# Kernel optimization log

Hardware: AMD Instinct MI355X
Metric: run time of the kernel (lower is better)

Reference implementation:

```python
import jax, jax.numpy as jnp
import numpy as np

E = 512; NH = 8; P = 4; Q = 900; CAMS = 7; DEPTH = 4
GRID = (480, 1440); IMG = (1080, 1920); FH = 68; FW = 120
NEG = -1e9  # stand-in for -inf in masked attention (avoids NaN on fully-masked rows)


def _ln(x, g, b):
    m = x.mean(-1, keepdims=True)
    v = jnp.mean((x - m) ** 2, -1, keepdims=True)
    return (x - m) / jnp.sqrt(v + 1e-5) * g + b


def _mlp2(x, w1, b1, w2, b2):
    return jax.nn.relu(x @ w1.T + b1) @ w2.T + b2


def _inv_sig(x, eps=1e-5):
    x = jnp.clip(x, 0.0, 1.0)
    return jnp.log(jnp.clip(x, eps, None) / jnp.clip(1.0 - x, eps, None))


def _mha(x, in_w, in_b, out_w, out_b, nh, mask=None):
    # x: [B, L, E]; mask: bool [B, nh, L, S], True = disallowed (torch semantics)
    B, L, Edim = x.shape
    d = Edim // nh
    qkv = x @ in_w.T + in_b
    q, k, v = jnp.split(qkv, 3, axis=-1)
    q = q.reshape(B, L, nh, d); k = k.reshape(B, L, nh, d); v = v.reshape(B, L, nh, d)
    s = jnp.einsum('blhd,bshd->bhls', q, k) * (1.0 / d ** 0.5)
    if mask is not None:
        s = jnp.where(mask, NEG, s)
    a = jax.nn.softmax(s, -1)
    o = jnp.einsum('bhls,bshd->blhd', a, v).reshape(B, L, Edim)
    return o @ out_w.T + out_b


def _grid_sample(feat, grid):
    # torch.F.grid_sample, bilinear, align_corners=False, zero padding
    # feat: [N, C, H, W], grid: [N, Pn, 2] in [-1, 1] -> [N, C, Pn]
    N, C, H, W = feat.shape
    x = (grid[..., 0] + 1.0) * (W / 2.0) - 0.5
    y = (grid[..., 1] + 1.0) * (H / 2.0) - 0.5
    x0f = jnp.floor(x); y0f = jnp.floor(y)
    wx1 = x - x0f; wy1 = y - y0f
    x0 = x0f.astype(jnp.int32); y0 = y0f.astype(jnp.int32)

    def gat(f, yi, xi):
        ok = ((yi >= 0) & (yi < H) & (xi >= 0) & (xi < W)).astype(f.dtype)
        return f[:, jnp.clip(yi, 0, H - 1), jnp.clip(xi, 0, W - 1)] * ok[None]

    def one(f, x0, y0, wx1, wy1):
        x1 = x0 + 1; y1 = y0 + 1
        wx0 = 1.0 - wx1; wy0 = 1.0 - wy1
        return (gat(f, y0, x0) * (wy0 * wx0)[None] + gat(f, y0, x1) * (wy0 * wx1)[None]
                + gat(f, y1, x0) * (wy1 * wx0)[None] + gat(f, y1, x1) * (wy1 * wx1)[None])

    return jax.vmap(one)(feat, x0, y0, wx1, wy1)


def _forward(img_feats, proj_mat, query, query_pos, reference_points, mha_in_w, mha_in_b, mha_out_w, mha_out_b, off_w1, off_b1, off_w2, off_b2, am_w1, am_b1, am_w2, am_b2, t_ln1_g, t_ln1_b, t_in_w, t_in_b, t_out_w, t_out_b, t_ln2_g, t_ln2_b, t_ff_w1, t_ff_b1, t_ff_w2, t_ff_b2, ffn_w1, ffn_b1, ffn_w2, ffn_b2, op_w, op_b, pe_w1, pe_bias1, pe_ln1_g, pe_ln1_b, pe_w2, pe_bias2, pe_ln2_g, pe_ln2_b, ln1_g, ln1_b, ln2_g, ln2_b, ln3_g, ln3_b):
    q = query + query_pos                                     # [Q, E]
    a = _mha(q[None], mha_in_w, mha_in_b, mha_out_w, mha_out_b, NH)[0]
    qn = _ln(a + q, ln1_g, ln1_b)
    offset = _mlp2(qn, off_w1, off_b1, off_w2, off_b2).reshape(-1, 2)   # [Q*P, 2]
    # torch: inverse_sigmoid(ref).repeat(4,1) + offset  (tile semantics preserved)
    rp_d = jax.nn.sigmoid(jnp.tile(_inv_sig(reference_points), (P, 1)) + offset)
    attn_w = jax.nn.softmax(_mlp2(qn, am_w1, am_b1, am_w2, am_b2), axis=-1)  # [Q, P]

    # --- feature_sampling ---
    scale = jnp.array([GRID[0], GRID[1]], rp_d.dtype)
    pts = jnp.concatenate([rp_d * scale, jnp.ones((Q * P, 1), rp_d.dtype)], -1)  # [Q*P, 3]
    ic = jnp.einsum('nij,pj->npi', proj_mat[0], pts)          # [CAMS, Q*P, 3]
    z = ic[..., 2]
    xy = ic[..., :2] / jnp.maximum(z, 1e-5)[..., None]
    cam = jnp.stack([(xy[..., 0] / IMG[1] - 0.5) * 2.0,
                     (xy[..., 1] / IMG[0] - 0.5) * 2.0], -1)  # [CAMS, Q*P, 2]
    valid = (z > 1e-5) & (cam[..., 0] > -1) & (cam[..., 0] < 1) & (cam[..., 1] > -1) & (cam[..., 1] < 1)
    mask = valid.reshape(CAMS, 1, Q, P).transpose(3, 2, 1, 0)  # [P, Q, 1, CAMS]
    sampled = _grid_sample(img_feats, cam)                    # [CAMS, E, Q*P]
    x = jnp.nan_to_num(sampled.transpose(2, 0, 1))            # [Q*P, CAMS, E]

    inv = ~mask
    m = jnp.tile(jnp.tile(inv, (1, NH, 1, 1)), (1, 1, CAMS, 1)).reshape(-1, CAMS, CAMS)
    mask4 = m.reshape(Q * P, NH, CAMS, CAMS)  # torch (batch*heads, L, S) layout

    for i in range(DEPTH):  # ImgFeatureTransformer, depth=4
        a = _mha(_ln(x, t_ln1_g[i], t_ln1_b[i]), t_in_w[i], t_in_b[i], t_out_w[i], t_out_b[i], NH, mask4)
        x = a + x
        x = _mlp2(_ln(x, t_ln2_g[i], t_ln2_b[i]), t_ff_w1[i], t_ff_b1[i], t_ff_w2[i], t_ff_b2[i]) + x

    out = (x.mean(1).reshape(Q, P, E) * attn_w[:, :, None]).mean(1) @ op_w.T + op_b
    pe = jax.nn.relu(_ln(_inv_sig(reference_points) @ pe_w1.T + pe_bias1, pe_ln1_g, pe_ln1_b))
    pe = jax.nn.relu(_ln(pe @ pe_w2.T + pe_bias2, pe_ln2_g, pe_ln2_b))
    qf = _ln(out + qn + pe, ln2_g, ln2_b)
    return _ln(_mlp2(qf, ffn_w1, ffn_b1, ffn_w2, ffn_b2) + qf, ln3_g, ln3_b)


def setup_inputs() -> dict:
    key = jax.random.key(0)
    ks = iter(jax.random.split(key, 80))
    def nrm(shape, s=1.0):
        return jax.random.normal(next(ks), shape, jnp.float32) * s
    def xw(shape):
        s = (2.0 / (shape[-1] + shape[-2])) ** 0.5
        return nrm(shape, s)
    rng = np.random.RandomState(0)
    base = np.array([[4.0, 0.0, 0.0], [0.0, 0.75, 0.0], [0.0, 0.0, 1.0]], np.float32)
    mats = []
    for _ in range(CAMS):
        M = base.copy()
        M[:2, :2] *= (1.0 + 0.1 * rng.randn(2, 2)).astype(np.float32)
        M[:2, 2] = (50.0 * rng.randn(2)).astype(np.float32)
        M[2, :2] = (1e-4 * rng.randn(2)).astype(np.float32)
        mats.append(M)
    return dict(
        img_feats=nrm((CAMS, E, FH, FW)),
        proj_mat=jnp.asarray(np.stack(mats))[None],
        query=nrm((Q, E), 0.1),
        query_pos=nrm((Q, E), 0.1),
        reference_points=jax.random.uniform(next(ks), (Q, 2), jnp.float32),
        mha_in_w=xw((3 * E, E)), mha_in_b=jnp.zeros((3 * E,)),
        mha_out_w=xw((E, E)), mha_out_b=jnp.zeros((E,)),
        off_w1=xw((E, E)), off_b1=jnp.zeros((E,)), off_w2=xw((2 * P, E)), off_b2=jnp.zeros((2 * P,)),
        am_w1=xw((E, E)), am_b1=jnp.zeros((E,)), am_w2=xw((P, E)), am_b2=jnp.zeros((P,)),
        t_ln1_g=jnp.ones((DEPTH, E)), t_ln1_b=jnp.zeros((DEPTH, E)),
        t_in_w=xw((DEPTH, 3 * E, E)), t_in_b=jnp.zeros((DEPTH, 3 * E)),
        t_out_w=xw((DEPTH, E, E)), t_out_b=jnp.zeros((DEPTH, E)),
        t_ln2_g=jnp.ones((DEPTH, E)), t_ln2_b=jnp.zeros((DEPTH, E)),
        t_ff_w1=xw((DEPTH, E, E)), t_ff_b1=jnp.zeros((DEPTH, E)),
        t_ff_w2=xw((DEPTH, E, E)), t_ff_b2=jnp.zeros((DEPTH, E)),
        ffn_w1=xw((E, E)), ffn_b1=jnp.zeros((E,)), ffn_w2=xw((E, E)), ffn_b2=jnp.zeros((E,)),
        op_w=xw((E, E)), op_b=jnp.zeros((E,)),
        pe_w1=xw((E, 2)), pe_bias1=jnp.zeros((E,)), pe_ln1_g=jnp.ones((E,)), pe_ln1_b=jnp.zeros((E,)),
        pe_w2=xw((E, E)), pe_bias2=jnp.zeros((E,)), pe_ln2_g=jnp.ones((E,)), pe_ln2_b=jnp.zeros((E,)),
        ln1_g=jnp.ones((E,)), ln1_b=jnp.zeros((E,)),
        ln2_g=jnp.ones((E,)), ln2_b=jnp.zeros((E,)),
        ln3_g=jnp.ones((E,)), ln3_b=jnp.zeros((E,)),
    )


def reference(img_feats, proj_mat, query, query_pos, reference_points, mha_in_w, mha_in_b, mha_out_w, mha_out_b, off_w1, off_b1, off_w2, off_b2, am_w1, am_b1, am_w2, am_b2, t_ln1_g, t_ln1_b, t_in_w, t_in_b, t_out_w, t_out_b, t_ln2_g, t_ln2_b, t_ff_w1, t_ff_b1, t_ff_w2, t_ff_b2, ffn_w1, ffn_b1, ffn_w2, ffn_b2, op_w, op_b, pe_w1, pe_bias1, pe_ln1_g, pe_ln1_b, pe_w2, pe_bias2, pe_ln2_g, pe_ln2_b, ln1_g, ln1_b, ln2_g, ln2_b, ln3_g, ln3_b):
    return _forward(img_feats, proj_mat, query, query_pos, reference_points, mha_in_w, mha_in_b, mha_out_w, mha_out_b, off_w1, off_b1, off_w2, off_b2, am_w1, am_b1, am_w2, am_b2, t_ln1_g, t_ln1_b, t_in_w, t_in_b, t_out_w, t_out_b, t_ln2_g, t_ln2_b, t_ff_w1, t_ff_b1, t_ff_w2, t_ff_b2, ffn_w1, ffn_b1, ffn_w2, ffn_b2, op_w, op_b, pe_w1, pe_bias1, pe_ln1_g, pe_ln1_b, pe_w2, pe_bias2, pe_ln2_g, pe_ln2_b, ln1_g, ln1_b, ln2_g, ln2_b, ln3_g, ln3_b)
```

## Files before the change

kernel.cpp:

```cpp
#include <hip/hip_runtime.h>
#include <hip/hip_bf16.h>

#define DEVI __device__ __forceinline__

typedef __bf16 bf16x8 __attribute__((ext_vector_type(8)));
typedef float f32x4 __attribute__((ext_vector_type(4)));

#define GLDS(gp, lp) __builtin_amdgcn_global_load_lds( \
    (const __attribute__((address_space(1))) void*)(gp), \
    (__attribute__((address_space(3))) void*)(lp), 16, 0, 0)

DEVI float b2f(ushort u) { unsigned v = ((unsigned)u) << 16; return __builtin_bit_cast(float, v); }
DEVI ushort f2bu(float x) { __hip_bfloat16 h = __float2bfloat16(x); return __builtin_bit_cast(ushort, h); }

__global__ __launch_bounds__(256) void gemm_mfma_k(
    const ushort* __restrict__ Ah, const ushort* __restrict__ Wh,
    const float* __restrict__ bias, const float* Rp,
    float* Cf, ushort* Cb,
    int M, int N, int K, int flags)
{
  __shared__ ushort As[128 * 32];
  __shared__ ushort Bs[128 * 32];
  const int tid = threadIdx.x;
  const int lane = tid & 63;
  const int wid = tid >> 6;
  const int bn = blockIdx.x * 128;
  const int bm = blockIdx.y * 128;
  const int wr = wid >> 1, wc = wid & 1;
  const int col = lane & 15;
  const int ksl = lane >> 4;
  const int sr = lane >> 2;
  const int sd = lane & 3;

  f32x4 acc[4][4];
#pragma unroll
  for (int m = 0; m < 4; ++m)
#pragma unroll
    for (int n = 0; n < 4; ++n) acc[m][n] = (f32x4){0.f, 0.f, 0.f, 0.f};

  for (int k0 = 0; k0 < K; k0 += 32) {
#pragma unroll
    for (int j = 0; j < 2; ++j) {
      const int r = wid * 32 + j * 16 + sr;
      const int ss = sd ^ (r & 3);
      GLDS(Ah + (long long)(bm + r) * K + k0 + ss * 8, &As[(wid * 32 + j * 16) * 32]);
      GLDS(Wh + (long long)(bn + r) * K + k0 + ss * 8, &Bs[(wid * 32 + j * 16) * 32]);
    }
    __syncthreads();
    bf16x8 af[4], bf[4];
#pragma unroll
    for (int m = 0; m < 4; ++m) {
      const int r = wr * 64 + m * 16 + col;
      af[m] = *(const bf16x8*)&As[r * 32 + ((ksl ^ (r & 3)) << 3)];
    }
#pragma unroll
    for (int n = 0; n < 4; ++n) {
      const int r = wc * 64 + n * 16 + col;
      bf[n] = *(const bf16x8*)&Bs[r * 32 + ((ksl ^ (r & 3)) << 3)];
    }
#pragma unroll
    for (int m = 0; m < 4; ++m)
#pragma unroll
      for (int n = 0; n < 4; ++n)
        acc[m][n] = __builtin_amdgcn_mfma_f32_16x16x32_bf16(af[m], bf[n], acc[m][n], 0, 0, 0);
    __syncthreads();
  }

  const int r4 = (lane >> 4) * 4;
#pragma unroll
  for (int m = 0; m < 4; ++m) {
#pragma unroll
    for (int j = 0; j < 4; ++j) {
      const int row = bm + wr * 64 + m * 16 + r4 + j;
      if (row >= M) continue;
#pragma unroll
      for (int n = 0; n < 4; ++n) {
        const int cn = bn + wc * 64 + n * 16 + col;
        float v = acc[m][n][j];
        if (flags & 1) v += bias[cn];
        if (flags & 2) v = fmaxf(v, 0.f);
        if (flags & 4) v += Rp[(long long)row * N + cn];
        if (flags & 8) Cb[(long long)row * N + cn] = f2bu(v);
        else           Cf[(long long)row * N + cn] = v;
      }
    }
  }
}

__global__ __launch_bounds__(256) void gemm_k(
    const float* __restrict__ Ap, long long a_base, int a_rs, int a_cs, long long a_zs,
    const float* __restrict__ Wp, long long w_base, int w_rs, int w_cs, long long w_zs,
    const float* __restrict__ bias,
    const float* Rp, int r_rs, long long r_zs,
    float* Cp, long long c_base, int c_rs, long long c_zs,
    int M, int N, int K, float alpha, int flags)
{
  __shared__ float As[8][132];
  __shared__ float Bs[8][132];
  const int z = blockIdx.z;
  const float* A = Ap + a_base + (long long)z * a_zs;
  const float* W = Wp + w_base + (long long)z * w_zs;
  float* C = Cp + c_base + (long long)z * c_zs;
  const float* R = (flags & 4) ? (Rp + (long long)z * r_zs) : nullptr;

  const int bm = blockIdx.y * 128;
  const int bn = blockIdx.x * 128;
  const int tid = threadIdx.x;
  const int tx = tid & 15;
  const int ty = tid >> 4;
  const int srow = tid >> 1;
  const int k4 = (tid & 1) * 4;

  float acc[8][8];
#pragma unroll
  for (int i = 0; i < 8; ++i)
#pragma unroll
    for (int j = 0; j < 8; ++j) acc[i][j] = 0.f;

  const int am = bm + srow;
  const int wn = bn + srow;
  const bool am_ok = am < M;
  const bool wn_ok = wn < N;
  const long long aoff = (long long)(am_ok ? am : 0) * a_rs;
  const long long woff = (long long)(wn_ok ? wn : 0) * w_rs;

  for (int k0 = 0; k0 < K; k0 += 8) {
    if (a_cs == 1 && am_ok && (k0 + 8 <= K)) {
      float4 v = *(const float4*)(A + aoff + k0 + k4);
      As[k4+0][srow] = v.x; As[k4+1][srow] = v.y;
      As[k4+2][srow] = v.z; As[k4+3][srow] = v.w;
    } else {
#pragma unroll
      for (int j = 0; j < 4; ++j) {
        int kk = k0 + k4 + j;
        float va = 0.f;
        if (am_ok && kk < K) va = A[aoff + (long long)kk * a_cs];
        As[k4+j][srow] = va;
      }
    }
    if (w_cs == 1 && wn_ok && (k0 + 8 <= K)) {
      float4 v = *(const float4*)(W + woff + k0 + k4);
      Bs[k4+0][srow] = v.x; Bs[k4+1][srow] = v.y;
      Bs[k4+2][srow] = v.z; Bs[k4+3][srow] = v.w;
    } else {
#pragma unroll
      for (int j = 0; j < 4; ++j) {
        int kk = k0 + k4 + j;
        float vb = 0.f;
        if (wn_ok && kk < K) vb = W[woff + (long long)kk * w_cs];
        Bs[k4+j][srow] = vb;
      }
    }
    __syncthreads();
#pragma unroll
    for (int kk = 0; kk < 8; ++kk) {
      float af[8], bf[8];
      *(float4*)&af[0] = *(const float4*)&As[kk][ty*8];
      *(float4*)&af[4] = *(const float4*)&As[kk][ty*8+4];
      *(float4*)&bf[0] = *(const float4*)&Bs[kk][tx*4];
      *(float4*)&bf[4] = *(const float4*)&Bs[kk][64+tx*4];
#pragma unroll
      for (int i = 0; i < 8; ++i)
#pragma unroll
        for (int j = 0; j < 8; ++j)
          acc[i][j] = fmaf(af[i], bf[j], acc[i][j]);
    }
    __syncthreads();
  }

#pragma unroll
  for (int i = 0; i < 8; ++i) {
    int m = bm + ty*8 + i;
    if (m >= M) continue;
#pragma unroll
    for (int jg = 0; jg < 2; ++jg) {
#pragma unroll
      for (int j = 0; j < 4; ++j) {
        int n = bn + jg*64 + tx*4 + j;
        if (n >= N) continue;
        float v = acc[i][jg*4+j] * alpha;
        if (flags & 1) v += bias[n];
        if (flags & 2) v = fmaxf(v, 0.f);
        if (flags & 4) v += R[(long long)m * r_rs + n];
        C[(long long)m * c_rs + n] = v;
      }
    }
  }
}

__global__ __launch_bounds__(256) void gemm_sk_k(
    const float* __restrict__ Ap, long long a_base, int a_rs, int a_cs, long long a_zs,
    const float* __restrict__ Wp, long long w_base, int w_rs, int w_cs, long long w_zs,
    float* __restrict__ P,
    int M, int N, int K, int KS)
{
  __shared__ float As[8][132];
  __shared__ float Bs[8][132];
  const int zks = blockIdx.z;
  const int z = zks / KS, ks = zks % KS;
  const int klen = (K + KS - 1) / KS;
  const int kbeg = ks * klen;
  const int kend = min(K, kbeg + klen);
  const float* A = Ap + a_base + (long long)z * a_zs;
  const float* W = Wp + w_base + (long long)z * w_zs;

  const int bm = blockIdx.y * 128;
  const int bn = blockIdx.x * 128;
  const int tid = threadIdx.x;
  const int tx = tid & 15;
  const int ty = tid >> 4;
  const int srow = tid >> 1;
  const int k4 = (tid & 1) * 4;

  float acc[8][8];
#pragma unroll
  for (int i = 0; i < 8; ++i)
#pragma unroll
    for (int j = 0; j < 8; ++j) acc[i][j] = 0.f;

  const int am = bm + srow;
  const int wn = bn + srow;
  const bool am_ok = am < M;
  const bool wn_ok = wn < N;
  const long long aoff = (long long)(am_ok ? am : 0) * a_rs;
  const long long woff = (long long)(wn_ok ? wn : 0) * w_rs;

  for (int k0 = kbeg; k0 < kend; k0 += 8) {
    if (a_cs == 1 && am_ok && (k0 + 8 <= kend)) {
      float4 v = *(const float4*)(A + aoff + k0 + k4);
      As[k4+0][srow] = v.x; As[k4+1][srow] = v.y;
      As[k4+2][srow] = v.z; As[k4+3][srow] = v.w;
    } else {
#pragma unroll
      for (int j = 0; j < 4; ++j) {
        int kk = k0 + k4 + j;
        float va = 0.f;
        if (am_ok && kk < kend) va = A[aoff + (long long)kk * a_cs];
        As[k4+j][srow] = va;
      }
    }
    if (w_cs == 1 && wn_ok && (k0 + 8 <= kend)) {
      float4 v = *(const float4*)(W + woff + k0 + k4);
      Bs[k4+0][srow] = v.x; Bs[k4+1][srow] = v.y;
      Bs[k4+2][srow] = v.z; Bs[k4+3][srow] = v.w;
    } else {
#pragma unroll
      for (int j = 0; j < 4; ++j) {
        int kk = k0 + k4 + j;
        float vb = 0.f;
        if (wn_ok && kk < kend) vb = W[woff + (long long)kk * w_cs];
        Bs[k4+j][srow] = vb;
      }
    }
    __syncthreads();
#pragma unroll
    for (int kk = 0; kk < 8; ++kk) {
      float af[8], bf[8];
      *(float4*)&af[0] = *(const float4*)&As[kk][ty*8];
      *(float4*)&af[4] = *(const float4*)&As[kk][ty*8+4];
      *(float4*)&bf[0] = *(const float4*)&Bs[kk][tx*4];
      *(float4*)&bf[4] = *(const float4*)&Bs[kk][64+tx*4];
#pragma unroll
      for (int i = 0; i < 8; ++i)
#pragma unroll
        for (int j = 0; j < 8; ++j)
          acc[i][j] = fmaf(af[i], bf[j], acc[i][j]);
    }
    __syncthreads();
  }

  float* Pz = P + ((long long)zks * M) * N;
#pragma unroll
  for (int i = 0; i < 8; ++i) {
    int m = bm + ty*8 + i;
    if (m >= M) continue;
#pragma unroll
    for (int jg = 0; jg < 2; ++jg) {
#pragma unroll
      for (int j = 0; j < 4; ++j) {
        int n = bn + jg*64 + tx*4 + j;
        if (n >= N) continue;
        Pz[(long long)m * N + n] = acc[i][jg*4+j];
      }
    }
  }
}

__global__ __launch_bounds__(256) void sk_reduce_k(
    const float* __restrict__ P, int M, int N, int KS, float alpha,
    const float* __restrict__ bias, const float* Rp, int r_rs, long long r_zs,
    float* Cp, long long c_base, int c_rs, long long c_zs, int flags)
{
  long long idx = (long long)blockIdx.x * 256 + threadIdx.x;
  if (idx >= (long long)M * N) return;
  const int z = blockIdx.y;
  const int m = (int)(idx / N), n = (int)(idx % N);
  const long long mn = (long long)M * N;
  const float* p = P + (long long)z * KS * mn + idx;
  float s = 0.f;
  for (int ks = 0; ks < KS; ++ks) s += p[(long long)ks * mn];
  s *= alpha;
  if (flags & 1) s += bias[n];
  if (flags & 2) s = fmaxf(s, 0.f);
  if (flags & 4) s += Rp[(long long)z * r_zs + (long long)m * r_rs + n];
  Cp[c_base + (long long)z * c_zs + (long long)m * c_rs + n] = s;
}

__global__ __launch_bounds__(256) void head_k(
    const float* __restrict__ A, const float* __restrict__ W,
    const float* __restrict__ bias, float* __restrict__ out, int N)
{
  __shared__ float red[4][8];
  const int m = blockIdx.x;
  const int tid = threadIdx.x, lane = tid & 63, w = tid >> 6;
  const float a0 = A[(long long)m * 512 + tid];
  const float a1 = A[(long long)m * 512 + tid + 256];
  for (int n = 0; n < N; ++n) {
    float p = a0 * W[n*512 + tid] + a1 * W[n*512 + tid + 256];
#pragma unroll
    for (int off = 32; off > 0; off >>= 1) p += __shfl_down(p, off, 64);
    if (lane == 0) red[w][n] = p;
  }
  __syncthreads();
  if (tid < N) out[(long long)m * N + tid] = red[0][tid]+red[1][tid]+red[2][tid]+red[3][tid] + bias[tid];
}

__global__ __launch_bounds__(256) void ln_k(
    const float* __restrict__ in0, const float* __restrict__ in1, const float* __restrict__ in2,
    const float* __restrict__ g, const float* __restrict__ b,
    float* __restrict__ outp, ushort* __restrict__ outb, int relu)
{
  __shared__ float red[8];
  const long long base = (long long)blockIdx.x * 512;
  const int tid = threadIdx.x;
  float x0 = in0[base + tid];
  float x1 = in0[base + tid + 256];
  if (in1) { x0 += in1[base + tid]; x1 += in1[base + tid + 256]; }
  if (in2) { x0 += in2[base + tid]; x1 += in2[base + tid + 256]; }
  float s = x0 + x1, q = x0*x0 + x1*x1;
#pragma unroll
  for (int off = 32; off > 0; off >>= 1) {
    s += __shfl_down(s, off, 64);
    q += __shfl_down(q, off, 64);
  }
  if ((tid & 63) == 0) { red[tid >> 6] = s; red[4 + (tid >> 6)] = q; }
  __syncthreads();
  if (tid == 0) {
    float S = red[0]+red[1]+red[2]+red[3];
    float Q = red[4]+red[5]+red[6]+red[7];
    float m = S * (1.f/512.f);
    float v = Q * (1.f/512.f) - m*m;
    red[0] = m; red[1] = rsqrtf(v + 1e-5f);
  }
  __syncthreads();
  float m = red[0], inv = red[1];
  float y0 = (x0 - m) * inv * g[tid]     + b[tid];
  float y1 = (x1 - m) * inv * g[tid+256] + b[tid+256];
  if (relu) { y0 = fmaxf(y0, 0.f); y1 = fmaxf(y1, 0.f); }
  if (outp) {
    outp[base + tid]       = y0;
    outp[base + tid + 256] = y1;
  }
  if (outb) {
    outb[base + tid]       = f2bu(y0);
    outb[base + tid + 256] = f2bu(y1);
  }
}

__global__ __launch_bounds__(256) void softmax_k(float* __restrict__ p, int S)
{
  __shared__ float red[8];
  float* r = p + (long long)blockIdx.x * S;
  const int tid = threadIdx.x;
  float vals[4];
  int cnt = 0;
  float mx = -3.0e38f;
  for (int e = tid; e < S; e += 256) { float v = r[e]; vals[cnt++] = v; mx = fmaxf(mx, v); }
#pragma unroll
  for (int off = 32; off > 0; off >>= 1) mx = fmaxf(mx, __shfl_down(mx, off, 64));
  if ((tid & 63) == 0) red[tid >> 6] = mx;
  __syncthreads();
  if (tid == 0) red[0] = fmaxf(fmaxf(red[0], red[1]), fmaxf(red[2], red[3]));
  __syncthreads();
  mx = red[0];
  float sum = 0.f;
  for (int i = 0; i < cnt; ++i) { vals[i] = expf(vals[i] - mx); sum += vals[i]; }
#pragma unroll
  for (int off = 32; off > 0; off >>= 1) sum += __shfl_down(sum, off, 64);
  if ((tid & 63) == 0) red[4 + (tid >> 6)] = sum;
  __syncthreads();
  if (tid == 0) red[4] = red[4]+red[5]+red[6]+red[7];
  __syncthreads();
  float inv = 1.f / red[4];
  cnt = 0;
  for (int e = tid; e < S; e += 256) r[e] = vals[cnt++] * inv;
}

__global__ __launch_bounds__(256) void softmax4_k(float* __restrict__ p, int rows)
{
  int i = blockIdx.x * 256 + threadIdx.x;
  if (i >= rows) return;
  float* r = p + (long long)i * 4;
  float m = fmaxf(fmaxf(r[0], r[1]), fmaxf(r[2], r[3]));
  float e0 = expf(r[0]-m), e1 = expf(r[1]-m), e2 = expf(r[2]-m), e3 = expf(r[3]-m);
  float inv = 1.f / (e0+e1+e2+e3);
  r[0] = e0*inv; r[1] = e1*inv; r[2] = e2*inv; r[3] = e3*inv;
}

__global__ __launch_bounds__(256) void add2_k(
    const float* __restrict__ a, const float* __restrict__ b, float* __restrict__ o, int n)
{
  int i = blockIdx.x * 256 + threadIdx.x;
  if (i < n) o[i] = a[i] + b[i];
}

__global__ __launch_bounds__(256) void f2b_k(
    const float* __restrict__ in, ushort* __restrict__ out, int n)
{
  int i = blockIdx.x * 256 + threadIdx.x;
  if (i < n) out[i] = f2bu(in[i]);
}

DEVI float inv_sig(float x)
{
  x = fminf(fmaxf(x, 0.f), 1.f);
  float a = fmaxf(x, 1e-5f);
  float c = fmaxf(1.f - x, 1e-5f);
  return logf(a / c);
}

__global__ __launch_bounds__(256) void sample_prep_k(
    const float* __restrict__ ref, const float* __restrict__ offs,
    const float* __restrict__ proj, float* __restrict__ camxy, float* __restrict__ valid)
{
  int n = blockIdx.x * 256 + threadIdx.x;
  if (n >= 3600) return;
  int qq = n >> 2, pp = n & 3;
  int rrow = n % 900;
  float tx = inv_sig(ref[rrow*2+0]) + offs[qq*8 + pp*2 + 0];
  float ty = inv_sig(ref[rrow*2+1]) + offs[qq*8 + pp*2 + 1];
  float sx = 1.f / (1.f + expf(-tx));
  float sy = 1.f / (1.f + expf(-ty));
  float px = sx * 480.f, py = sy * 1440.f;
#pragma unroll
  for (int c = 0; c < 7; ++c) {
    const float* M = proj + c*9;
    float icx = M[0]*px + M[1]*py + M[2];
    float icy = M[3]*px + M[4]*py + M[5];
    float icz = M[6]*px + M[7]*py + M[8];
    float zc = fmaxf(icz, 1e-5f);
    float cx = (icx/zc/1920.f - 0.5f) * 2.f;
    float cy = (icy/zc/1080.f - 0.5f) * 2.f;
    int ok = (icz > 1e-5f) && (cx > -1.f) && (cx < 1.f) && (cy > -1.f) && (cy < 1.f);
    camxy[((long long)c*3600+n)*2+0] = cx;
    camxy[((long long)c*3600+n)*2+1] = cy;
    valid[(long long)c*3600+n] = ok ? 1.f : 0.f;
  }
}

__global__ __launch_bounds__(256) void timg_k(
    const float* __restrict__ img, ushort* __restrict__ out)
{
  __shared__ float t[32][33];
  const int cam = blockIdx.z;
  const int hw0 = blockIdx.x * 32;
  const int c0  = blockIdx.y * 32;
  const int tx = threadIdx.x & 31, ty = threadIdx.x >> 5;
  const float* src = img + ((long long)cam * 512 + c0) * 8160 + hw0;
#pragma unroll
  for (int i = 0; i < 4; ++i)
    t[ty + i*8][tx] = src[(long long)(ty + i*8) * 8160 + tx];
  __syncthreads();
  ushort* dst = out + ((long long)cam * 8160 + hw0) * 512 + c0;
#pragma unroll
  for (int i = 0; i < 4; ++i)
    dst[(long long)(ty + i*8) * 512 + tx] = f2bu(t[tx][ty + i*8]);
}

__global__ __launch_bounds__(128) void grid_sample2_k(
    const ushort* __restrict__ imgT, const float* __restrict__ camxy,
    float* __restrict__ xout)
{
  const int blk = blockIdx.x;
  const int pt = blk / 7, cam = blk % 7;
  float gx = camxy[((long long)cam*3600+pt)*2+0];
  float gy = camxy[((long long)cam*3600+pt)*2+1];
  float fx = (gx + 1.f) * 60.f - 0.5f;
  float fy = (gy + 1.f) * 34.f - 0.5f;
  float x0f = floorf(fx), y0f = floorf(fy);
  float wx1 = fx - x0f, wy1 = fy - y0f;
  float wx0 = 1.f - wx1, wy0 = 1.f - wy1;
  x0f = fminf(fmaxf(x0f, -2.e9f), 2.e9f);
  y0f = fminf(fmaxf(y0f, -2.e9f), 2.e9f);
  int x0 = (int)x0f, y0 = (int)y0f;
  int x1 = x0 + 1, y1 = y0 + 1;
  bool okx0 = (x0 >= 0) && (x0 < 120);
  bool okx1 = (x1 >= 0) && (x1 < 120);
  bool oky0 = (y0 >= 0) && (y0 < 68);
  bool oky1 = (y1 >= 0) && (y1 < 68);
  int cx0 = min(max(x0,0),119), cx1 = min(max(x1,0),119);
  int cy0 = min(max(y0,0),67),  cy1 = min(max(y1,0),67);
  float w00 = (okx0 && oky0) ? wy0*wx0 : 0.f;
  float w01 = (okx1 && oky0) ? wy0*wx1 : 0.f;
  float w10 = (okx0 && oky1) ? wy1*wx0 : 0.f;
  float w11 = (okx1 && oky1) ? wy1*wx1 : 0.f;
  const long long i00 = (long long)(cy0*120+cx0) * 512;
  const long long i01 = (long long)(cy0*120+cx1) * 512;
  const long long i10 = (long long)(cy1*120+cx0) * 512;
  const long long i11 = (long long)(cy1*120+cx1) * 512;
  const ushort* f = imgT + (long long)cam * 8160 * 512;
  float* o = xout + (long long)blk * 512;
  const int c = threadIdx.x * 4;
  ushort4 u00 = *(const ushort4*)(f + i00 + c);
  ushort4 u01 = *(const ushort4*)(f + i01 + c);
  ushort4 u10 = *(const ushort4*)(f + i10 + c);
  ushort4 u11 = *(const ushort4*)(f + i11 + c);
  float4 r;
  r.x = b2f(u00.x)*w00 + b2f(u01.x)*w01 + b2f(u10.x)*w10 + b2f(u11.x)*w11;
  r.y = b2f(u00.y)*w00 + b2f(u01.y)*w01 + b2f(u10.y)*w10 + b2f(u11.y)*w11;
  r.z = b2f(u00.z)*w00 + b2f(u01.z)*w01 + b2f(u10.z)*w10 + b2f(u11.z)*w11;
  r.w = b2f(u00.w)*w00 + b2f(u01.w)*w01 + b2f(u10.w)*w10 + b2f(u11.w)*w11;
  *(float4*)(o + c) = r;
}

__global__ __launch_bounds__(256) void tf_attn_k(
    const float* __restrict__ qkv, const float* __restrict__ valid,
    ushort* __restrict__ outp, int batch0)
{
  __shared__ float sv[7*1536];
  const int lb = blockIdx.x;
  const int ib = batch0 + lb;
  const float4* src = (const float4*)(qkv + (long long)lb * (7*1536));
  float4* dst4 = (float4*)sv;
  for (int idx = threadIdx.x; idx < 7*1536/4; idx += 256) dst4[idx] = src[idx];
  __syncthreads();
  const int tid = threadIdx.x;
  if (tid < 56) {
    const int h = tid / 7, sq = tid % 7;
    const int bb = ib*8 + h;
    const int pp = bb / 7200;
    const int rr = (bb - pp*7200) % 900;
    const float* qrow = sv + sq*1536 + h*64;
    float sc[7];
    float mx = -3.0e38f;
#pragma unroll
    for (int t = 0; t < 7; ++t) {
      const float* krow = sv + t*1536 + 512 + h*64;
      float d = 0.f;
      for (int e = 0; e < 64; ++e) d = fmaf(qrow[e], krow[e], d);
      d *= 0.125f;
      if (valid[(long long)t*3600 + rr*4 + pp] == 0.f) d = -1e9f;
      sc[t] = d;
      mx = fmaxf(mx, d);
    }
    float sum = 0.f;
#pragma unroll
    for (int t = 0; t < 7; ++t) { sc[t] = expf(sc[t] - mx); sum += sc[t]; }
    float inv = 1.f / sum;
#pragma unroll
    for (int t = 0; t < 7; ++t) sc[t] *= inv;
    ushort* orow = outp + ((long long)ib*7 + sq)*512 + h*64;
    for (int e = 0; e < 64; e += 4) {
      float a0=0.f, a1=0.f, a2=0.f, a3=0.f;
#pragma unroll
      for (int t = 0; t < 7; ++t) {
        const float* vr = sv + t*1536 + 1024 + h*64 + e;
        float w = sc[t];
        a0 = fmaf(w, vr[0], a0); a1 = fmaf(w, vr[1], a1);
        a2 = fmaf(w, vr[2], a2); a3 = fmaf(w, vr[3], a3);
      }
      ushort4 st;
      st.x = f2bu(a0); st.y = f2bu(a1); st.z = f2bu(a2); st.w = f2bu(a3);
      *(ushort4*)orow = st;
      orow += 4;
    }
  }
}

__global__ __launch_bounds__(256) void pool_k(
    const float* __restrict__ x, const float* __restrict__ aw, ushort* __restrict__ o)
{
  int qq = blockIdx.x;
  for (int c = threadIdx.x; c < 512; c += 256) {
    float acc = 0.f;
#pragma unroll
    for (int p = 0; p < 4; ++p) {
      const float* xr = x + ((long long)(qq*4+p)*7)*512 + c;
      float s = 0.f;
#pragma unroll
      for (int cam = 0; cam < 7; ++cam) s += xr[cam*512];
      acc = fmaf(s, aw[qq*4+p], acc);
    }
    o[(long long)qq*512 + c] = f2bu(acc * (1.f/28.f));
  }
}

__global__ __launch_bounds__(256) void pe1_k(
    const float* __restrict__ ref, const float* __restrict__ w1, const float* __restrict__ b1,
    float* __restrict__ o)
{
  int idx = blockIdx.x * 256 + threadIdx.x;
  if (idx >= 900*512) return;
  int qq = idx >> 9, c = idx & 511;
  float i0 = inv_sig(ref[qq*2+0]);
  float i1 = inv_sig(ref[qq*2+1]);
  o[idx] = i0*w1[c*2+0] + i1*w1[c*2+1] + b1[c];
}

extern "C" void kernel_launch(void* const* d_in, const int* in_sizes, int n_in,
                              void* d_out, int out_size, void* d_ws, size_t ws_size,
                              hipStream_t stream)
{
  (void)in_sizes; (void)n_in; (void)out_size;
  const float* img      = (const float*)d_in[0];
  const float* proj     = (const float*)d_in[1];
  const float* query    = (const float*)d_in[2];
  const float* qpos     = (const float*)d_in[3];
  const float* ref      = (const float*)d_in[4];
  const float* mha_in_w = (const float*)d_in[5];
  const float* mha_in_b = (const float*)d_in[6];
  const float* mha_out_w= (const float*)d_in[7];
  const float* mha_out_b= (const float*)d_in[8];
  const float* off_w1   = (const float*)d_in[9];
  const float* off_b1   = (const float*)d_in[10];
  const float* off_w2   = (const float*)d_in[11];
  const float* off_b2   = (const float*)d_in[12];
  const float* am_w1    = (const float*)d_in[13];
  const float* am_b1    = (const float*)d_in[14];
  const float* am_w2    = (const float*)d_in[15];
  const float* am_b2    = (const float*)d_in[16];
  const float* t_ln1_g  = (const float*)d_in[17];
  const float* t_ln1_b  = (const float*)d_in[18];
  const float* t_in_w   = (const float*)d_in[19];
  const float* t_in_b   = (const float*)d_in[20];
  const float* t_out_w  = (const float*)d_in[21];
  const float* t_out_b  = (const float*)d_in[22];
  const float* t_ln2_g  = (const float*)d_in[23];
  const float* t_ln2_b  = (const float*)d_in[24];
  const float* t_ff_w1  = (const float*)d_in[25];
  const float* t_ff_b1  = (const float*)d_in[26];
  const float* t_ff_w2  = (const float*)d_in[27];
  const float* t_ff_b2  = (const float*)d_in[28];
  const float* ffn_w1   = (const float*)d_in[29];
  const float* ffn_b1   = (const float*)d_in[30];
  const float* ffn_w2   = (const float*)d_in[31];
  const float* ffn_b2   = (const float*)d_in[32];
  const float* op_w     = (const float*)d_in[33];
  const float* op_b     = (const float*)d_in[34];
  const float* pe_w1    = (const float*)d_in[35];
  const float* pe_bias1 = (const float*)d_in[36];
  const float* pe_ln1_g = (const float*)d_in[37];
  const float* pe_ln1_b = (const float*)d_in[38];
  const float* pe_w2    = (const float*)d_in[39];
  const float* pe_bias2 = (const float*)d_in[40];
  const float* pe_ln2_g = (const float*)d_in[41];
  const float* pe_ln2_b = (const float*)d_in[42];
  const float* ln1_g    = (const float*)d_in[43];
  const float* ln1_b    = (const float*)d_in[44];
  const float* ln2_g    = (const float*)d_in[45];
  const float* ln2_b    = (const float*)d_in[46];
  const float* ln3_g    = (const float*)d_in[47];
  const float* ln3_b    = (const float*)d_in[48];

  char* wsb = (char*)d_ws;
  size_t off = 0;
  auto alloc = [&](long long bytes) -> char* {
    char* p = wsb + off;
    off += (size_t)((bytes + 255) / 256 * 256);
    return p;
  };
  float* X    = (float*)alloc(25200ll * 512 * 4);
  float* QKV  = (float*)alloc(4200ll * 1536 * 4);
  char*  R1   = alloc(7ll * 8160 * 512 * 2);
  ushort* imgT = (ushort*)R1;
  ushort* XNh  = (ushort*)R1;
  ushort* Hh   = (ushort*)(R1 + 25344ll * 512 * 2);
  ushort* Wqkvh = (ushort*)alloc(4ll * 1536 * 512 * 2);
  ushort* Wouth = (ushort*)alloc(4ll * 512 * 512 * 2);
  ushort* Wff1h = (ushort*)alloc(4ll * 512 * 512 * 2);
  ushort* Wff2h = (ushort*)alloc(4ll * 512 * 512 * 2);
  ushort* Wtailh = (ushort*)alloc(4ll * 512 * 512 * 2);
  ushort* PoolH = (ushort*)alloc(1024ll * 512 * 2);
  ushort* PEh   = (ushort*)alloc(1024ll * 512 * 2);
  ushort* S3h   = (ushort*)alloc(1024ll * 512 * 2);
  ushort* Hh2   = (ushort*)alloc(1024ll * 512 * 2);
  float* S0   = (float*)alloc(900ll * 512 * 4);
  float* S1   = (float*)alloc(900ll * 512 * 4);
  float* S2   = (float*)alloc(900ll * 512 * 4);
  float* S3   = (float*)alloc(900ll * 512 * 4);
  float* S4   = (float*)alloc(900ll * 512 * 4);
  float* S5   = (float*)alloc(900ll * 512 * 4);
  float* OFFB = (float*)alloc(900ll * 8 * 4);
  float* AMB  = (float*)alloc(900ll * 4 * 4);
  float* CXY  = (float*)alloc(7ll * 3600 * 2 * 4);
  float* VAL  = (float*)alloc(7ll * 3600 * 4);
  if (off > ws_size) return;

  float* SC  = X;
  float* P1  = X;
  float* P2  = X + 6500000;
  float* QKV1 = QKV;

  auto gemm = [&](const float* A, long long ab, int ars, int acs, long long azs,
                  const float* W, long long wb, int wrs, int wcs, long long wzs,
                  const float* bias, const float* R, int rrs, long long rzs,
                  float* C, long long cb, int crs, long long czs,
                  int M, int N, int K, float alpha, int flags, int Z) {
    dim3 grd((unsigned)((N + 127) / 128), (unsigned)((M + 127) / 128), (unsigned)Z);
    gemm_k<<<grd, dim3(256), 0, stream>>>(A, ab, ars, acs, azs, W, wb, wrs, wcs, wzs,
                                          bias, R, rrs, rzs, C, cb, crs, czs,
                                          M, N, K, alpha, flags);
  };
  auto skgemm = [&](const float* A, long long ab, int ars, int acs, long long azs,
                    const float* W, long long wb, int wrs, int wcs, long long wzs,
                    float* P, const float* bias, const float* R, int rrs, long long rzs,
                    float* C, long long cb, int crs, long long czs,
                    int M, int N, int K, float alpha, int flags, int Z, int KS) {
    dim3 grd((unsigned)((N + 127) / 128), (unsigned)((M + 127) / 128), (unsigned)(Z * KS));
    gemm_sk_k<<<grd, dim3(256), 0, stream>>>(A, ab, ars, acs, azs, W, wb, wrs, wcs, wzs,
                                             P, M, N, K, KS);
    dim3 grd2((unsigned)(((long long)M * N + 255) / 256), (unsigned)Z);
    sk_reduce_k<<<grd2, dim3(256), 0, stream>>>(P, M, N, KS, alpha, bias, R, rrs, rzs,
                                                C, cb, crs, czs, flags);
  };
  auto mgemm = [&](const ushort* A, const ushort* W, const float* bias,
                   const float* R, float* Cf, ushort* Cb,
                   int M, int N, int K, int flags) {
    dim3 grd((unsigned)(N / 128), (unsigned)((M + 127) / 128), 1);
    gemm_mfma_k<<<grd, dim3(256), 0, stream>>>(A, W, bias, R, Cf, Cb, M, N, K, flags);
  };

  f2b_k<<<(4*1536*512+255)/256, 256, 0, stream>>>(t_in_w,  Wqkvh, 4*1536*512);
  f2b_k<<<(4*512*512+255)/256, 256, 0, stream>>>(t_out_w, Wouth, 4*512*512);
  f2b_k<<<(4*512*512+255)/256, 256, 0, stream>>>(t_ff_w1, Wff1h, 4*512*512);
  f2b_k<<<(4*512*512+255)/256, 256, 0, stream>>>(t_ff_w2, Wff2h, 4*512*512);
  f2b_k<<<(512*512+255)/256, 256, 0, stream>>>(op_w,   Wtailh + 0ll*512*512, 512*512);
  f2b_k<<<(512*512+255)/256, 256, 0, stream>>>(pe_w2,  Wtailh + 1ll*512*512, 512*512);
  f2b_k<<<(512*512+255)/256, 256, 0, stream>>>(ffn_w1, Wtailh + 2ll*512*512, 512*512);
  f2b_k<<<(512*512+255)/256, 256, 0, stream>>>(ffn_w2, Wtailh + 3ll*512*512, 512*512);
  timg_k<<<dim3(255, 16, 7), 256, 0, stream>>>(img, imgT);

  add2_k<<<1800, 256, 0, stream>>>(query, qpos, S0, 460800);
  skgemm(S0,0,512,1,0,  mha_in_w,0,512,1,0,  P1, mha_in_b, nullptr,0,0,
         QKV1,0,1536,0,  900,1536,512, 1.f, 1, 1, 8);
  gemm(QKV1,0,1536,1,64,  QKV1,512,1536,1,64,  nullptr, nullptr,0,0,
       SC,0,900,810000,  900,900,64, 0.125f, 0, 8);
  softmax_k<<<7200, 256, 0, stream>>>(SC, 900);
  skgemm(SC,0,900,1,810000,  QKV1,1024,1,1536,64,  P2, nullptr, nullptr,0,0,
         S1,0,512,64,  900,64,900, 1.f, 0, 8, 8);
  skgemm(S1,0,512,1,0,  mha_out_w,0,512,1,0,  P2, mha_out_b, S0,512,0,
         S2,0,512,0,  900,512,512, 1.f, 1|4, 1, 8);
  ln_k<<<900, 256, 0, stream>>>(S2, nullptr, nullptr, ln1_g, ln1_b, S1, nullptr, 0);

  skgemm(S1,0,512,1,0, off_w1,0,512,1,0, P2, off_b1, nullptr,0,0,
         S2,0,512,0, 900,512,512, 1.f, 1|2, 1, 8);
  head_k<<<900, 256, 0, stream>>>(S2, off_w2, off_b2, OFFB, 8);
  skgemm(S1,0,512,1,0, am_w1,0,512,1,0, P2, am_b1, nullptr,0,0,
         S2,0,512,0, 900,512,512, 1.f, 1|2, 1, 8);
  head_k<<<900, 256, 0, stream>>>(S2, am_w2, am_b2, AMB, 4);
  softmax4_k<<<4, 256, 0, stream>>>(AMB, 900);

  sample_prep_k<<<15, 256, 0, stream>>>(ref, OFFB, proj, CXY, VAL);
  grid_sample2_k<<<25200, 128, 0, stream>>>(imgT, CXY, X);

  for (int L = 0; L < 4; ++L) {
    const float* g1  = t_ln1_g + L*512;  const float* bb1 = t_ln1_b + L*512;
    const float* bq  = t_in_b + L*1536;
    const float* bo  = t_out_b + L*512;
    const float* g2  = t_ln2_g + L*512;  const float* bb2 = t_ln2_b + L*512;
    const float* f1  = t_ff_b1 + L*512;
    const float* f2  = t_ff_b2 + L*512;
    const ushort* wq = Wqkvh + (long long)L*1536*512;
    const ushort* wo = Wouth + (long long)L*512*512;
    const ushort* w1 = Wff1h + (long long)L*512*512;
    const ushort* w2 = Wff2h + (long long)L*512*512;

    ln_k<<<25200, 256, 0, stream>>>(X, nullptr, nullptr, g1, bb1, nullptr, XNh, 0);
    for (int ch = 0; ch < 6; ++ch) {
      mgemm(XNh + (long long)ch*4200*512, wq, bq, nullptr, QKV, nullptr,
            4200, 1536, 512, 1);
      tf_attn_k<<<600, 256, 0, stream>>>(QKV, VAL, XNh, ch*600);
    }
    mgemm(XNh, wo, bo, X, X, nullptr, 25200, 512, 512, 1|4);
    ln_k<<<25200, 256, 0, stream>>>(X, nullptr, nullptr, g2, bb2, nullptr, XNh, 0);
    mgemm(XNh, w1, f1, nullptr, nullptr, Hh, 25200, 512, 512, 1|2|8);
    mgemm(Hh, w2, f2, X, X, nullptr, 25200, 512, 512, 1|4);
  }

  pool_k<<<900, 256, 0, stream>>>(X, AMB, PoolH);
  mgemm(PoolH, Wtailh + 0ll*512*512, op_b, nullptr, S4, nullptr, 900, 512, 512, 1);
  pe1_k<<<1800, 256, 0, stream>>>(ref, pe_w1, pe_bias1, S2);
  ln_k<<<900, 256, 0, stream>>>(S2, nullptr, nullptr, pe_ln1_g, pe_ln1_b, nullptr, PEh, 1);
  mgemm(PEh, Wtailh + 1ll*512*512, pe_bias2, nullptr, S2, nullptr, 900, 512, 512, 1);
  ln_k<<<900, 256, 0, stream>>>(S2, nullptr, nullptr, pe_ln2_g, pe_ln2_b, S5, nullptr, 1);
  ln_k<<<900, 256, 0, stream>>>(S4, S1, S5, ln2_g, ln2_b, S3, S3h, 0);
  mgemm(S3h, Wtailh + 2ll*512*512, ffn_b1, nullptr, nullptr, Hh2, 900, 512, 512, 1|2|8);
  mgemm(Hh2, Wtailh + 3ll*512*512, ffn_b2, S3, S4, nullptr, 900, 512, 512, 1|4);
  ln_k<<<900, 256, 0, stream>>>(S4, nullptr, nullptr, ln3_g, ln3_b, (float*)d_out, nullptr, 0);
}
```

Before: 2.894 ms.

## Double-buffer MFMA GEMM LDS tiles and store QKV in bf16 for attention

The bf16 MFMA GEMM now keeps two LDS buffers and issues the global-to-LDS loads for the next K tile before computing the current one, with one barrier per iteration instead of two. This aims to hide global load latency behind the MFMA work, at the cost of twice the LDS per block, which may lower occupancy. Separately, the QKV projection output is written as bf16 instead of fp32, and the attention kernel reads bf16 and converts to float. This halves QKV write and read traffic and the LDS footprint of the attention kernel, but adds bf16 rounding to q, k and v.

```diff
diff --git a/kernel.cpp b/kernel.cpp
--- a/kernel.cpp
+++ b/kernel.cpp
@@ -19,8 +19,8 @@
     float* Cf, ushort* Cb,
     int M, int N, int K, int flags)
 {
-  __shared__ ushort As[128 * 32];
-  __shared__ ushort Bs[128 * 32];
+  __shared__ ushort As[2][128 * 32];
+  __shared__ ushort Bs[2][128 * 32];
   const int tid = threadIdx.x;
   const int lane = tid & 63;
   const int wid = tid >> 6;
@@ -29,8 +29,6 @@
   const int wr = wid >> 1, wc = wid & 1;
   const int col = lane & 15;
   const int ksl = lane >> 4;
-  const int sr = lane >> 2;
-  const int sd = lane & 3;
 
   f32x4 acc[4][4];
 #pragma unroll
@@ -38,33 +36,45 @@
 #pragma unroll
     for (int n = 0; n < 4; ++n) acc[m][n] = (f32x4){0.f, 0.f, 0.f, 0.f};
 
-  for (int k0 = 0; k0 < K; k0 += 32) {
+  auto stage = [&](int buf, int t) {
 #pragma unroll
     for (int j = 0; j < 2; ++j) {
-      const int r = wid * 32 + j * 16 + sr;
-      const int ss = sd ^ (r & 3);
-      GLDS(Ah + (long long)(bm + r) * K + k0 + ss * 8, &As[(wid * 32 + j * 16) * 32]);
-      GLDS(Wh + (long long)(bn + r) * K + k0 + ss * 8, &Bs[(wid * 32 + j * 16) * 32]);
-    }
-    __syncthreads();
+      const int r = wid * 32 + j * 16 + (lane >> 2);
+      const int ss = (lane & 3) ^ (r & 3);
+      GLDS(Ah + (long long)(bm + r) * K + t * 32 + ss * 8, &As[buf][(wid * 32 + j * 16) * 32]);
+      GLDS(Wh + (long long)(bn + r) * K + t * 32 + ss * 8, &Bs[buf][(wid * 32 + j * 16) * 32]);
+    }
+  };
+  auto compute = [&](int buf) {
     bf16x8 af[4], bf[4];
 #pragma unroll
     for (int m = 0; m < 4; ++m) {
       const int r = wr * 64 + m * 16 + col;
-      af[m] = *(const bf16x8*)&As[r * 32 + ((ksl ^ (r & 3)) << 3)];
+      af[m] = *(const bf16x8*)&As[buf][r * 32 + ((ksl ^ (r & 3)) << 3)];
     }
 #pragma unroll
     for (int n = 0; n < 4; ++n) {
       const int r = wc * 64 + n * 16 + col;
-      bf[n] = *(const bf16x8*)&Bs[r * 32 + ((ksl ^ (r & 3)) << 3)];
+      bf[n] = *(const bf16x8*)&Bs[buf][r * 32 + ((ksl ^ (r & 3)) << 3)];
     }
 #pragma unroll
     for (int m = 0; m < 4; ++m)
 #pragma unroll
       for (int n = 0; n < 4; ++n)
         acc[m][n] = __builtin_amdgcn_mfma_f32_16x16x32_bf16(af[m], bf[n], acc[m][n], 0, 0, 0);
+  };
+
+  const int nt = K >> 5;
+  stage(0, 0);
+  __syncthreads();
+  int cur = 0;
+  for (int t = 0; t < nt - 1; ++t) {
+    stage(cur ^ 1, t + 1);
+    compute(cur);
     __syncthreads();
-  }
+    cur ^= 1;
+  }
+  compute(cur);
 
   const int r4 = (lane >> 4) * 4;
 #pragma unroll
@@ -524,15 +534,15 @@
 }
 
 __global__ __launch_bounds__(256) void tf_attn_k(
-    const float* __restrict__ qkv, const float* __restrict__ valid,
+    const ushort* __restrict__ qkv, const float* __restrict__ valid,
     ushort* __restrict__ outp, int batch0)
 {
-  __shared__ float sv[7*1536];
+  __shared__ ushort sv[7*1536];
   const int lb = blockIdx.x;
   const int ib = batch0 + lb;
-  const float4* src = (const float4*)(qkv + (long long)lb * (7*1536));
-  float4* dst4 = (float4*)sv;
-  for (int idx = threadIdx.x; idx < 7*1536/4; idx += 256) dst4[idx] = src[idx];
+  const uint4* src = (const uint4*)(qkv + (long long)lb * (7*1536));
+  uint4* dst4 = (uint4*)sv;
+  for (int idx = threadIdx.x; idx < 7*1536/8; idx += 256) dst4[idx] = src[idx];
   __syncthreads();
   const int tid = threadIdx.x;
   if (tid < 56) {
@@ -540,14 +550,30 @@
     const int bb = ib*8 + h;
     const int pp = bb / 7200;
     const int rr = (bb - pp*7200) % 900;
-    const float* qrow = sv + sq*1536 + h*64;
+    float qv[64];
+    {
+      const ushort* qrow = sv + sq*1536 + h*64;
+#pragma unroll
+      for (int e4 = 0; e4 < 16; ++e4) {
+        ushort4 u = *(const ushort4*)(qrow + e4*4);
+        qv[e4*4+0] = b2f(u.x); qv[e4*4+1] = b2f(u.y);
+        qv[e4*4+2] = b2f(u.z); qv[e4*4+3] = b2f(u.w);
+      }
+    }
     float sc[7];
     float mx = -3.0e38f;
 #pragma unroll
     for (int t = 0; t < 7; ++t) {
-      const float* krow = sv + t*1536 + 512 + h*64;
+      const ushort* krow = sv + t*1536 + 512 + h*64;
       float d = 0.f;
-      for (int e = 0; e < 64; ++e) d = fmaf(qrow[e], krow[e], d);
+#pragma unroll
+      for (int e4 = 0; e4 < 16; ++e4) {
+        ushort4 u = *(const ushort4*)(krow + e4*4);
+        d = fmaf(qv[e4*4+0], b2f(u.x), d);
+        d = fmaf(qv[e4*4+1], b2f(u.y), d);
+        d = fmaf(qv[e4*4+2], b2f(u.z), d);
+        d = fmaf(qv[e4*4+3], b2f(u.w), d);
+      }
       d *= 0.125f;
       if (valid[(long long)t*3600 + rr*4 + pp] == 0.f) d = -1e9f;
       sc[t] = d;
@@ -564,10 +590,10 @@
       float a0=0.f, a1=0.f, a2=0.f, a3=0.f;
 #pragma unroll
       for (int t = 0; t < 7; ++t) {
-        const float* vr = sv + t*1536 + 1024 + h*64 + e;
+        ushort4 u = *(const ushort4*)(sv + t*1536 + 1024 + h*64 + e);
         float w = sc[t];
-        a0 = fmaf(w, vr[0], a0); a1 = fmaf(w, vr[1], a1);
-        a2 = fmaf(w, vr[2], a2); a3 = fmaf(w, vr[3], a3);
+        a0 = fmaf(w, b2f(u.x), a0); a1 = fmaf(w, b2f(u.y), a1);
+        a2 = fmaf(w, b2f(u.z), a2); a3 = fmaf(w, b2f(u.w), a3);
       }
       ushort4 st;
       st.x = f2bu(a0); st.y = f2bu(a1); st.z = f2bu(a2); st.w = f2bu(a3);
@@ -700,6 +726,7 @@
   float* P1  = X;
   float* P2  = X + 6500000;
   float* QKV1 = QKV;
+  ushort* QKVh = (ushort*)QKV;
 
   auto gemm = [&](const float* A, long long ab, int ars, int acs, long long azs,
                   const float* W, long long wb, int wrs, int wcs, long long wzs,
@@ -777,9 +804,9 @@
 
     ln_k<<<25200, 256, 0, stream>>>(X, nullptr, nullptr, g1, bb1, nullptr, XNh, 0);
     for (int ch = 0; ch < 6; ++ch) {
-      mgemm(XNh + (long long)ch*4200*512, wq, bq, nullptr, QKV, nullptr,
-            4200, 1536, 512, 1);
-      tf_attn_k<<<600, 256, 0, stream>>>(QKV, VAL, XNh, ch*600);
+      mgemm(XNh + (long long)ch*4200*512, wq, bq, nullptr, nullptr, QKVh,
+            4200, 1536, 512, 1|8);
+      tf_attn_k<<<600, 256, 0, stream>>>(QKVh, VAL, XNh, ch*600);
     }
     mgemm(XNh, wo, bo, X, X, nullptr, 25200, 512, 512, 1|4);
     ln_k<<<25200, 256, 0, stream>>>(X, nullptr, nullptr, g2, bb2, nullptr, XNh, 0);
```

After: 2.839 ms. No clear change (-1.9%).
